# Performance work log

Hardware: AMD Instinct MI355X
Metric: run time of the kernel (lower is better)

Reference implementation:

```python
import jax, jax.numpy as jnp
import numpy as np

B, NF, E, T, M = 4096, 50, 64, 2, 3
LN_EPS = 1e-5
NEG_INF = -1e9


def _xavier_uniform(k, shape, fan_in, fan_out):
    a = float(np.sqrt(6.0 / (fan_in + fan_out)))
    return jax.random.uniform(k, shape, jnp.float32, -a, a)


def setup_inputs() -> dict:
    key = jax.random.key(0)
    ks = jax.random.split(key, 6)
    feat = jax.random.normal(ks[0], (B, NF, E), jnp.float32)
    masker = _xavier_uniform(ks[1], (T, M, NF, NF), NF, NF)
    transform_w = _xavier_uniform(ks[2], (1, T, 1, 2 * E, E), 2 * E, E)
    transform_b = _xavier_uniform(ks[3], (T, 1, NF, E), NF, E)
    ln_w = jnp.ones((NF,), jnp.float32)
    ln_b = jnp.zeros((NF,), jnp.float32)
    gating_w = jax.random.normal(ks[4], (NF * E, 1), jnp.float32) / np.sqrt(NF * E)
    gating_b = jnp.zeros((1,), jnp.float32)
    return {
        "feat": feat,
        "masker": masker,
        "transform_w": transform_w,
        "transform_b": transform_b,
        "ln_w": ln_w,
        "ln_b": ln_b,
        "gating_w": gating_w,
        "gating_b": gating_b,
    }


def reference(feat, masker, transform_w, transform_b, ln_w, ln_b, gating_w, gating_b):
    b, nf, e = feat.shape
    t = masker.shape[0]
    # hop adjacency: product of masks, relu'd  (T, F, F)
    adj = jax.nn.relu(jnp.prod(masker, axis=1))
    mask = (adj != 0).astype(feat.dtype)
    # LayerNorm(num_fields) applied on transposed adj == normalize over axis -2,
    # with gamma/beta broadcasting along the normalized (row) axis.
    mean = adj.mean(axis=-2, keepdims=True)
    var = adj.var(axis=-2, keepdims=True)
    adj_ln = (adj - mean) / jnp.sqrt(var + LN_EPS) * ln_w[:, None] + ln_b[:, None]
    logits = adj_ln + (1.0 - mask) * NEG_INF + jnp.eye(nf, dtype=feat.dtype)
    # softmax over dim=1 of (T, F, F) == axis -2 (rows), then re-mask
    attn = jax.nn.softmax(logits, axis=-2) * mask
    # nei[b,t,g,e] = sum_f feat[b,f,e] * attn[t,f,g]
    nei = jnp.einsum('bfe,tfg->btge', feat, attn)  # (B, T, F, E)
    x = jnp.broadcast_to(feat[:, None], (b, t, nf, e))
    cat = jnp.concatenate([x, nei], axis=-1)  # (B, T, F, 2E)
    w0 = transform_w[0, :, 0]                 # (T, 2E, E)  (idx=0 slice)
    h = jnp.einsum('btfk,tke->btfe', cat, w0) + transform_b[:, 0]  # (B,T,F,E)
    flat = h.reshape(b, t, nf * e)
    gate = jax.nn.softmax(flat @ gating_w + gating_b, axis=1)  # (B, T, 1)
    out = jnp.sum(flat * gate, axis=1).reshape(b, nf, e)
    return out
```

## Files before the change

kernel.cpp:

```cpp
#include <hip/hip_runtime.h>
#include <hip/hip_bf16.h>

#define NFEAT 50
#define EDIM 64
#define LN_EPS 1e-5f
#define NEG_INF_C (-1000000000.0f)
#define NB 4

typedef __bf16 bf16_t;
typedef __bf16 bf16x8 __attribute__((ext_vector_type(8)));
typedef __bf16 bf16x4 __attribute__((ext_vector_type(4)));
typedef float f32x4 __attribute__((ext_vector_type(4)));


__global__ __launch_bounds__(256) void prep_kernel(
    const float* __restrict__ masker, const float* __restrict__ ln_w,
    const float* __restrict__ ln_b, const float* __restrict__ tw,
    bf16_t* __restrict__ ws_attnT, bf16_t* __restrict__ ws_WT)
{
  const int tid = threadIdx.x;
  const int lane = tid & 63;

  const int gidx = blockIdx.x * 256 + tid;
#pragma unroll
  for (int j = 0; j < 4; ++j) {
    int o = gidx * 4 + j;
    int k = o & 63;
    int e = (o >> 6) & 63;
    int ti = o >> 12;
    ws_WT[o] = (bf16_t)tw[(ti * 64 + k) * 64 + e];
  }

  const int wg = blockIdx.x * 4 + (tid >> 6);
  const int f = lane;
  const bool fv = (f < NFEAT);
  for (int i = 0; i < 2; ++i) {
    int col = wg * 2 + i;
    int t = col >> 6, g = col & 63;
    float val = 0.f;
    if (fv && g < NFEAT) {
      float a0 = masker[((t * 3 + 0) * NFEAT + f) * NFEAT + g];
      float a1 = masker[((t * 3 + 1) * NFEAT + f) * NFEAT + g];
      float a2 = masker[((t * 3 + 2) * NFEAT + f) * NFEAT + g];
      float prod = a0 * a1 * a2;
      val = prod > 0.f ? prod : 0.f;
    }
    float s = val;
    for (int off = 32; off > 0; off >>= 1) s += __shfl_xor(s, off);
    float mean = s / (float)NFEAT;
    float d = fv ? (val - mean) : 0.f;
    float v2 = d * d;
    for (int off = 32; off > 0; off >>= 1) v2 += __shfl_xor(v2, off);
    float var = v2 / (float)NFEAT;
    float lw = fv ? ln_w[f] : 0.f;
    float lb = fv ? ln_b[f] : 0.f;
    float aln = d * rsqrtf(var + LN_EPS) * lw + lb;
    float logit = aln + ((val != 0.f) ? 0.f : NEG_INF_C) + ((f == g) ? 1.f : 0.f);
    if (!fv) logit = -3.0e38f;
    float mx = logit;
    for (int off = 32; off > 0; off >>= 1) mx = fmaxf(mx, __shfl_xor(mx, off));
    float ex = fv ? expf(logit - mx) : 0.f;
    float se = ex;
    for (int off = 32; off > 0; off >>= 1) se += __shfl_xor(se, off);
    float attn = (fv && g < NFEAT && val != 0.f) ? (ex / se) : 0.f;
    ws_attnT[(t * 64 + g) * 64 + f] = (bf16_t)attn;
  }
}

__global__ __launch_bounds__(256) void main_kernel(
    const float* __restrict__ feat, const float* __restrict__ tb,
    const float* __restrict__ gw, const float* __restrict__ gb,
    const bf16_t* __restrict__ ws_attnT, const bf16_t* __restrict__ ws_WT,
    float* __restrict__ out)
{
  __shared__ bf16_t sPT[2][64 * 72];
  __shared__ float sLog[2][4];

  const int tid = threadIdx.x;
  const int w = tid >> 6;
  const int lane = tid & 63;
  const int l16 = lane & 15;
  const int lquad = lane >> 4;
  const int m0 = w * 16;

  bf16x8 aat[2][2];
#pragma unroll
  for (int t = 0; t < 2; ++t)
#pragma unroll
    for (int kc = 0; kc < 2; ++kc)
      aat[t][kc] = *(const bf16x8*)(ws_attnT + (t * 64 + m0 + l16) * 64 + kc * 32 + lquad * 8);

  float tbr[2][4][4], gwr[4][4];
#pragma unroll
  for (int n = 0; n < 4; ++n) {
    int e = n * 16 + l16;
#pragma unroll
    for (int r = 0; r < 4; ++r) {
      int f = m0 + lquad * 4 + r;
      bool v = (f < NFEAT);
      gwr[n][r]    = v ? gw[f * 64 + e] : 0.f;
      tbr[0][n][r] = v ? tb[(0 * NFEAT + f) * 64 + e] : 0.f;
      tbr[1][n][r] = v ? tb[(1 * NFEAT + f) * 64 + e] : 0.f;
    }
  }
  const float gbv = gb[0];
  const int fA = m0 + l16;

  for (int ib = 0; ib < NB; ++ib) {
    const int b = blockIdx.x * NB + ib;
    const float* featb = feat + b * (NFEAT * EDIM);

    bf16x8 a[2];
#pragma unroll
    for (int kc = 0; kc < 2; ++kc) {
#pragma unroll
      for (int j = 0; j < 8; ++j) a[kc][j] = (bf16_t)0.f;
      if (fA < NFEAT) {
        const float4* pa = (const float4*)(featb + fA * 64 + kc * 32 + lquad * 8);
        float4 x0 = pa[0], x1 = pa[1];
        a[kc][0] = (bf16_t)x0.x; a[kc][1] = (bf16_t)x0.y; a[kc][2] = (bf16_t)x0.z; a[kc][3] = (bf16_t)x0.w;
        a[kc][4] = (bf16_t)x1.x; a[kc][5] = (bf16_t)x1.y; a[kc][6] = (bf16_t)x1.z; a[kc][7] = (bf16_t)x1.w;
      }
    }

    f32x4 accH[2][4], accP[2][4];
#pragma unroll
    for (int t = 0; t < 2; ++t)
#pragma unroll
      for (int n = 0; n < 4; ++n) {
        accH[t][n] = (f32x4){0.f, 0.f, 0.f, 0.f};
        accP[t][n] = (f32x4){0.f, 0.f, 0.f, 0.f};
      }

#pragma unroll
    for (int kc = 0; kc < 2; ++kc) {
#pragma unroll
      for (int n = 0; n < 4; ++n) {
        const int bo = (n * 16 + l16) * 64 + kc * 32 + lquad * 8;
        const bf16x8 b10 = *(const bf16x8*)(ws_WT + (0 * 64) * 64 + bo);
        const bf16x8 b20 = *(const bf16x8*)(ws_WT + (1 * 64) * 64 + bo);
        const bf16x8 b11 = *(const bf16x8*)(ws_WT + (2 * 64) * 64 + bo);
        const bf16x8 b21 = *(const bf16x8*)(ws_WT + (3 * 64) * 64 + bo);
        accH[0][n] = __builtin_amdgcn_mfma_f32_16x16x32_bf16(a[kc], b10, accH[0][n], 0, 0, 0);
        accP[0][n] = __builtin_amdgcn_mfma_f32_16x16x32_bf16(a[kc], b20, accP[0][n], 0, 0, 0);
        accH[1][n] = __builtin_amdgcn_mfma_f32_16x16x32_bf16(a[kc], b11, accH[1][n], 0, 0, 0);
        accP[1][n] = __builtin_amdgcn_mfma_f32_16x16x32_bf16(a[kc], b21, accP[1][n], 0, 0, 0);
      }
    }

#pragma unroll
    for (int t = 0; t < 2; ++t)
#pragma unroll
      for (int n = 0; n < 4; ++n) {
        bf16x4 pv;
        pv[0] = (bf16_t)accP[t][n][0]; pv[1] = (bf16_t)accP[t][n][1];
        pv[2] = (bf16_t)accP[t][n][2]; pv[3] = (bf16_t)accP[t][n][3];
        *(bf16x4*)&sPT[t][(n * 16 + l16) * 72 + m0 + lquad * 4] = pv;
      }
    __syncthreads();

#pragma unroll
    for (int kc = 0; kc < 2; ++kc) {
#pragma unroll
      for (int n = 0; n < 4; ++n) {
        const int so = (n * 16 + l16) * 72 + kc * 32 + lquad * 8;
        const bf16x8 bp0 = *(const bf16x8*)(&sPT[0][so]);
        const bf16x8 bp1 = *(const bf16x8*)(&sPT[1][so]);
        accH[0][n] = __builtin_amdgcn_mfma_f32_16x16x32_bf16(aat[0][kc], bp0, accH[0][n], 0, 0, 0);
        accH[1][n] = __builtin_amdgcn_mfma_f32_16x16x32_bf16(aat[1][kc], bp1, accH[1][n], 0, 0, 0);
      }
    }

    float p0 = 0.f, p1 = 0.f;
#pragma unroll
    for (int n = 0; n < 4; ++n)
#pragma unroll
      for (int r = 0; r < 4; ++r) {
        float h0 = accH[0][n][r] + tbr[0][n][r];
        float h1 = accH[1][n][r] + tbr[1][n][r];
        accH[0][n][r] = h0; accH[1][n][r] = h1;
        p0 += h0 * gwr[n][r];
        p1 += h1 * gwr[n][r];
      }
#pragma unroll
    for (int off = 32; off > 0; off >>= 1) {
      p0 += __shfl_xor(p0, off);
      p1 += __shfl_xor(p1, off);
    }
    if (lane == 0) { sLog[0][w] = p0; sLog[1][w] = p1; }
    __syncthreads();

    const float g0 = sLog[0][0] + sLog[0][1] + sLog[0][2] + sLog[0][3] + gbv;
    const float g1 = sLog[1][0] + sLog[1][1] + sLog[1][2] + sLog[1][3] + gbv;
    const float mx = fmaxf(g0, g1);
    const float e0 = expf(g0 - mx), e1 = expf(g1 - mx);
    const float inv = 1.f / (e0 + e1);
    const float ga0 = e0 * inv, ga1 = e1 * inv;

    float* outb = out + b * (NFEAT * EDIM);
#pragma unroll
    for (int n = 0; n < 4; ++n) {
      int e = n * 16 + l16;
#pragma unroll
      for (int r = 0; r < 4; ++r) {
        int f = m0 + lquad * 4 + r;
        if (f < NFEAT)
          outb[f * 64 + e] = ga0 * accH[0][n][r] + ga1 * accH[1][n][r];
      }
    }
  }
}

extern "C" void kernel_launch(void* const* d_in, const int* in_sizes, int n_in,
                              void* d_out, int out_size, void* d_ws, size_t ws_size,
                              hipStream_t stream) {
  const float* feat   = (const float*)d_in[0];
  const float* masker = (const float*)d_in[1];
  const float* tw     = (const float*)d_in[2];
  const float* tb     = (const float*)d_in[3];
  const float* lnw    = (const float*)d_in[4];
  const float* lnb    = (const float*)d_in[5];
  const float* gw     = (const float*)d_in[6];
  const float* gb     = (const float*)d_in[7];
  float* out = (float*)d_out;

  bf16_t* ws_attnT = (bf16_t*)d_ws;
  bf16_t* ws_WT    = ws_attnT + 2 * 64 * 64;

  prep_kernel<<<16, 256, 0, stream>>>(masker, lnw, lnb, tw, ws_attnT, ws_WT);
  main_kernel<<<4096 / NB, 256, 0, stream>>>(feat, tb, gw, gb, ws_attnT, ws_WT, out);
}
```

Measured before the change: 168.5 us.

## Cut register pressure with precomputed bias/gate constants and prefetch next feat

The prep kernel now writes transposed bias and gating weights to workspace and precomputes the constant gate-logit term (bias dotted with gating weights). The main kernel no longer keeps the bias, gating and attention fragments in registers across the batch loop. It reloads them per batch from workspace, declares launch bounds with a minimum of 4 blocks, and prefetches the next batch's feature row while computing the current one. The aim is higher occupancy and hidden global load latency, at the cost of extra per-iteration cached loads.

Result: slower. 378.8 us (+124.8%).

```diff
diff --git a/kernel.cpp b/kernel.cpp
--- a/kernel.cpp
+++ b/kernel.cpp
@@ -16,12 +16,16 @@
 __global__ __launch_bounds__(256) void prep_kernel(
     const float* __restrict__ masker, const float* __restrict__ ln_w,
     const float* __restrict__ ln_b, const float* __restrict__ tw,
-    bf16_t* __restrict__ ws_attnT, bf16_t* __restrict__ ws_WT)
+    const float* __restrict__ tb, const float* __restrict__ gw,
+    bf16_t* __restrict__ ws_attnT, bf16_t* __restrict__ ws_WT,
+    float* __restrict__ ws_tbT, float* __restrict__ ws_gwT,
+    float* __restrict__ ws_cst)
 {
+  __shared__ float red[2][4];
   const int tid = threadIdx.x;
   const int lane = tid & 63;
-
   const int gidx = blockIdx.x * 256 + tid;
+
 #pragma unroll
   for (int j = 0; j < 4; ++j) {
     int o = gidx * 4 + j;
@@ -29,6 +33,41 @@
     int e = (o >> 6) & 63;
     int ti = o >> 12;
     ws_WT[o] = (bf16_t)tw[(ti * 64 + k) * 64 + e];
+  }
+
+#pragma unroll
+  for (int j = 0; j < 2; ++j) {
+    int o = gidx * 2 + j;
+    int f = o & 63;
+    int e = (o >> 6) & 63;
+    int t = o >> 12;
+    ws_tbT[o] = (f < NFEAT) ? tb[(t * NFEAT + f) * EDIM + e] : 0.f;
+  }
+
+  {
+    int o = gidx;
+    int f = o & 63;
+    int e = o >> 6;
+    ws_gwT[o] = (f < NFEAT) ? gw[f * EDIM + e] : 0.f;
+  }
+
+  if (blockIdx.x == 0) {
+    float s0 = 0.f, s1 = 0.f;
+    for (int i = tid; i < NFEAT * EDIM; i += 256) {
+      float g = gw[i];
+      s0 += tb[i] * g;
+      s1 += tb[NFEAT * EDIM + i] * g;
+    }
+    for (int off = 32; off > 0; off >>= 1) {
+      s0 += __shfl_xor(s0, off);
+      s1 += __shfl_xor(s1, off);
+    }
+    if (lane == 0) { red[0][tid >> 6] = s0; red[1][tid >> 6] = s1; }
+    __syncthreads();
+    if (tid == 0) {
+      ws_cst[0] = red[0][0] + red[0][1] + red[0][2] + red[0][3];
+      ws_cst[1] = red[1][0] + red[1][1] + red[1][2] + red[1][3];
+    }
   }
 
   const int wg = blockIdx.x * 4 + (tid >> 6);
@@ -67,10 +106,11 @@
   }
 }
 
-__global__ __launch_bounds__(256) void main_kernel(
-    const float* __restrict__ feat, const float* __restrict__ tb,
-    const float* __restrict__ gw, const float* __restrict__ gb,
+__global__ __launch_bounds__(256, 4) void main_kernel(
+    const float* __restrict__ feat, const float* __restrict__ gb,
     const bf16_t* __restrict__ ws_attnT, const bf16_t* __restrict__ ws_WT,
+    const float* __restrict__ ws_tbT, const float* __restrict__ ws_gwT,
+    const float* __restrict__ ws_cst,
     float* __restrict__ out)
 {
   __shared__ bf16_t sPT[2][64 * 72];
@@ -83,44 +123,47 @@
   const int lquad = lane >> 4;
   const int m0 = w * 16;
 
-  bf16x8 aat[2][2];
-#pragma unroll
-  for (int t = 0; t < 2; ++t)
+  const float gbv = gb[0];
+  const float cst0 = ws_cst[0];
+  const float cst1 = ws_cst[1];
+  const int fA = m0 + l16;
+  const bool fAv = (fA < NFEAT);
+  const int b0 = blockIdx.x * NB;
+  const int featoff = fA * 64 + lquad * 8;
+
+  f32x4 raw[4];
+  if (fAv) {
+    const float* fb = feat + b0 * (NFEAT * EDIM) + featoff;
+    raw[0] = *(const f32x4*)(fb);
+    raw[1] = *(const f32x4*)(fb + 4);
+    raw[2] = *(const f32x4*)(fb + 32);
+    raw[3] = *(const f32x4*)(fb + 36);
+  }
+
+  for (int ib = 0; ib < NB; ++ib) {
+    const int b = b0 + ib;
+
+    bf16x8 a[2];
 #pragma unroll
     for (int kc = 0; kc < 2; ++kc)
-      aat[t][kc] = *(const bf16x8*)(ws_attnT + (t * 64 + m0 + l16) * 64 + kc * 32 + lquad * 8);
-
-  float tbr[2][4][4], gwr[4][4];
-#pragma unroll
-  for (int n = 0; n < 4; ++n) {
-    int e = n * 16 + l16;
-#pragma unroll
-    for (int r = 0; r < 4; ++r) {
-      int f = m0 + lquad * 4 + r;
-      bool v = (f < NFEAT);
-      gwr[n][r]    = v ? gw[f * 64 + e] : 0.f;
-      tbr[0][n][r] = v ? tb[(0 * NFEAT + f) * 64 + e] : 0.f;
-      tbr[1][n][r] = v ? tb[(1 * NFEAT + f) * 64 + e] : 0.f;
-    }
-  }
-  const float gbv = gb[0];
-  const int fA = m0 + l16;
-
-  for (int ib = 0; ib < NB; ++ib) {
-    const int b = blockIdx.x * NB + ib;
-    const float* featb = feat + b * (NFEAT * EDIM);
-
-    bf16x8 a[2];
-#pragma unroll
-    for (int kc = 0; kc < 2; ++kc) {
 #pragma unroll
       for (int j = 0; j < 8; ++j) a[kc][j] = (bf16_t)0.f;
-      if (fA < NFEAT) {
-        const float4* pa = (const float4*)(featb + fA * 64 + kc * 32 + lquad * 8);
-        float4 x0 = pa[0], x1 = pa[1];
-        a[kc][0] = (bf16_t)x0.x; a[kc][1] = (bf16_t)x0.y; a[kc][2] = (bf16_t)x0.z; a[kc][3] = (bf16_t)x0.w;
-        a[kc][4] = (bf16_t)x1.x; a[kc][5] = (bf16_t)x1.y; a[kc][6] = (bf16_t)x1.z; a[kc][7] = (bf16_t)x1.w;
-      }
+    if (fAv) {
+#pragma unroll
+      for (int kc = 0; kc < 2; ++kc)
+#pragma unroll
+        for (int j = 0; j < 4; ++j) {
+          a[kc][j]     = (bf16_t)raw[kc * 2][j];
+          a[kc][j + 4] = (bf16_t)raw[kc * 2 + 1][j];
+        }
+    }
+
+    if (ib + 1 < NB && fAv) {
+      const float* fb = feat + (b + 1) * (NFEAT * EDIM) + featoff;
+      raw[0] = *(const f32x4*)(fb);
+      raw[1] = *(const f32x4*)(fb + 4);
+      raw[2] = *(const f32x4*)(fb + 32);
+      raw[3] = *(const f32x4*)(fb + 36);
     }
 
     f32x4 accH[2][4], accP[2][4];
@@ -161,26 +204,30 @@
 
 #pragma unroll
     for (int kc = 0; kc < 2; ++kc) {
+      const bf16x8 aat0 = *(const bf16x8*)(ws_attnT + (0 * 64 + m0 + l16) * 64 + kc * 32 + lquad * 8);
+      const bf16x8 aat1 = *(const bf16x8*)(ws_attnT + (1 * 64 + m0 + l16) * 64 + kc * 32 + lquad * 8);
 #pragma unroll
       for (int n = 0; n < 4; ++n) {
         const int so = (n * 16 + l16) * 72 + kc * 32 + lquad * 8;
         const bf16x8 bp0 = *(const bf16x8*)(&sPT[0][so]);
         const bf16x8 bp1 = *(const bf16x8*)(&sPT[1][so]);
-        accH[0][n] = __builtin_amdgcn_mfma_f32_16x16x32_bf16(aat[0][kc], bp0, accH[0][n], 0, 0, 0);
-        accH[1][n] = __builtin_amdgcn_mfma_f32_16x16x32_bf16(aat[1][kc], bp1, accH[1][n], 0, 0, 0);
-      }
-    }
+        accH[0][n] = __builtin_amdgcn_mfma_f32_16x16x32_bf16(aat0, bp0, accH[0][n], 0, 0, 0);
+        accH[1][n] = __builtin_amdgcn_mfma_f32_16x16x32_bf16(aat1, bp1, accH[1][n], 0, 0, 0);
+      }
+    }
+
+    f32x4 gwv[4];
+#pragma unroll
+    for (int n = 0; n < 4; ++n)
+      gwv[n] = *(const f32x4*)(ws_gwT + (n * 16 + l16) * 64 + m0 + lquad * 4);
 
     float p0 = 0.f, p1 = 0.f;
 #pragma unroll
     for (int n = 0; n < 4; ++n)
 #pragma unroll
       for (int r = 0; r < 4; ++r) {
-        float h0 = accH[0][n][r] + tbr[0][n][r];
-        float h1 = accH[1][n][r] + tbr[1][n][r];
-        accH[0][n][r] = h0; accH[1][n][r] = h1;
-        p0 += h0 * gwr[n][r];
-        p1 += h1 * gwr[n][r];
+        p0 += accH[0][n][r] * gwv[n][r];
+        p1 += accH[1][n][r] * gwv[n][r];
       }
 #pragma unroll
     for (int off = 32; off > 0; off >>= 1) {
@@ -190,8 +237,16 @@
     if (lane == 0) { sLog[0][w] = p0; sLog[1][w] = p1; }
     __syncthreads();
 
-    const float g0 = sLog[0][0] + sLog[0][1] + sLog[0][2] + sLog[0][3] + gbv;
-    const float g1 = sLog[1][0] + sLog[1][1] + sLog[1][2] + sLog[1][3] + gbv;
+    f32x4 tbv0[4], tbv1[4];
+#pragma unroll
+    for (int n = 0; n < 4; ++n) {
+      const int ro = (n * 16 + l16) * 64 + m0 + lquad * 4;
+      tbv0[n] = *(const f32x4*)(ws_tbT + ro);
+      tbv1[n] = *(const f32x4*)(ws_tbT + 64 * 64 + ro);
+    }
+
+    const float g0 = sLog[0][0] + sLog[0][1] + sLog[0][2] + sLog[0][3] + cst0 + gbv;
+    const float g1 = sLog[1][0] + sLog[1][1] + sLog[1][2] + sLog[1][3] + cst1 + gbv;
     const float mx = fmaxf(g0, g1);
     const float e0 = expf(g0 - mx), e1 = expf(g1 - mx);
     const float inv = 1.f / (e0 + e1);
@@ -205,7 +260,8 @@
       for (int r = 0; r < 4; ++r) {
         int f = m0 + lquad * 4 + r;
         if (f < NFEAT)
-          outb[f * 64 + e] = ga0 * accH[0][n][r] + ga1 * accH[1][n][r];
+          outb[f * 64 + e] = ga0 * (accH[0][n][r] + tbv0[n][r])
+                           + ga1 * (accH[1][n][r] + tbv1[n][r]);
       }
     }
   }
@@ -226,7 +282,12 @@
 
   bf16_t* ws_attnT = (bf16_t*)d_ws;
   bf16_t* ws_WT    = ws_attnT + 2 * 64 * 64;
-
-  prep_kernel<<<16, 256, 0, stream>>>(masker, lnw, lnb, tw, ws_attnT, ws_WT);
-  main_kernel<<<4096 / NB, 256, 0, stream>>>(feat, tb, gw, gb, ws_attnT, ws_WT, out);
+  float*  ws_tbT   = (float*)(ws_WT + 4 * 64 * 64);
+  float*  ws_gwT   = ws_tbT + 2 * 64 * 64;
+  float*  ws_cst   = ws_gwT + 64 * 64;
+
+  prep_kernel<<<16, 256, 0, stream>>>(masker, lnw, lnb, tw, tb, gw,
+                                      ws_attnT, ws_WT, ws_tbT, ws_gwT, ws_cst);
+  main_kernel<<<4096 / NB, 256, 0, stream>>>(feat, gb, ws_attnT, ws_WT,
+                                             ws_tbT, ws_gwT, ws_cst, out);
 }
```
